# Performance work log

Hardware: AMD Instinct MI355X
Metric: run time of the kernel (lower is better)

## Reference

```python
import jax, jax.numpy as jnp
import numpy as np

B, S, D, H, F, REF = 4, 1024, 512, 8, 2048, 2
HGRID = 32   # sqrt(seq_len)
HALF = 3     # 7x7 window -> half-width 3


def _masks():
    i = jnp.arange(HGRID)
    near = jnp.abs(i[:, None] - i[None, :]) <= HALF            # [h,h]
    inside = (near[:, None, :, None] & near[None, :, None, :]).reshape(S, S)
    # reverse=True mask (mca): outside-window -> -inf, inside -> 0
    m_rev = jnp.where(inside, 0.0, -jnp.inf).astype(jnp.float32)
    # reverse=False mask (msa/nsa): inside-window -> -inf, outside -> 0 (faithful to source)
    m_fwd = jnp.where(inside, -jnp.inf, 0.0).astype(jnp.float32)
    return m_rev, m_fwd


def _mha(q, k, v, w, b, ow, ob, mask):
    # torch nn.MultiheadAttention, batch_first, eval mode (no dropout)
    hd = D // H
    wq, wk, wv = jnp.split(w, 3, axis=0)
    bq, bk, bv = jnp.split(b, 3)

    def proj(t, wt, bt):
        Bt, Lt = t.shape[0], t.shape[1]
        return (t @ wt.T + bt).reshape(Bt, Lt, H, hd).transpose(0, 2, 1, 3)

    qh, kh, vh = proj(q, wq, bq), proj(k, wk, bk), proj(v, wv, bv)
    scores = jnp.einsum('bhqd,bhkd->bhqk', qh, kh) / jnp.sqrt(jnp.float32(hd))
    if mask is not None:
        scores = scores + mask
    a = jax.nn.softmax(scores, axis=-1)
    o = jnp.einsum('bhqk,bhkd->bhqd', a, vh).transpose(0, 2, 1, 3).reshape(q.shape[0], q.shape[1], D)
    return o @ ow.T + ob


def _ln(x, g, b, eps=1e-5):
    m = x.mean(-1, keepdims=True)
    v = ((x - m) ** 2).mean(-1, keepdims=True)
    return (x - m) / jnp.sqrt(v + eps) * g + b


def setup_inputs() -> dict:
    key = jax.random.key(0)
    ks = jax.random.split(key, 16)
    d = {}
    d['x'] = jax.random.normal(ks[0], (B, S, D), jnp.float32)
    d['ref_mca'] = jax.random.normal(ks[1], (B, REF * S, D), jnp.float32)
    d['gate'] = jax.random.uniform(ks[2], (B, S, 5), jnp.float32)
    i = 3
    for p in ['mca', 'ca', 'msa', 'nsa', 'sa']:
        d[p + '_w'] = 0.02 * jax.random.normal(ks[i], (3 * D, D), jnp.float32); i += 1
        d[p + '_b'] = jnp.zeros((3 * D,), jnp.float32)
        d[p + '_ow'] = 0.02 * jax.random.normal(ks[i], (D, D), jnp.float32); i += 1
        d[p + '_ob'] = jnp.zeros((D,), jnp.float32)
    d['ln1_g'] = jnp.ones((D,), jnp.float32); d['ln1_b'] = jnp.zeros((D,), jnp.float32)
    d['ln2_g'] = jnp.ones((D,), jnp.float32); d['ln2_b'] = jnp.zeros((D,), jnp.float32)
    d['fc1_w'] = 0.02 * jax.random.normal(ks[i], (F, D), jnp.float32); i += 1
    d['fc1_b'] = jnp.zeros((F,), jnp.float32)
    d['fc2_w'] = 0.02 * jax.random.normal(ks[i], (D, F), jnp.float32); i += 1
    d['fc2_b'] = jnp.zeros((D,), jnp.float32)
    return d


def reference(x, ref_mca, gate,
              mca_w, mca_b, mca_ow, mca_ob,
              ca_w, ca_b, ca_ow, ca_ob,
              msa_w, msa_b, msa_ow, msa_ob,
              nsa_w, nsa_b, nsa_ow, nsa_ob,
              sa_w, sa_b, sa_ow, sa_ob,
              ln1_g, ln1_b, ln2_g, ln2_b,
              fc1_w, fc1_b, fc2_w, fc2_b):
    m_rev, m_fwd = _masks()
    # mca branch: sum attention over each seq_len chunk of ref_mca (window-inside mask)
    mca_x = jnp.zeros_like(x)
    for r in range(REF):
        chunk = ref_mca[:, r * S:(r + 1) * S, :]
        mca_x = mca_x + _mha(x, chunk, chunk, mca_w, mca_b, mca_ow, mca_ob, m_rev)
    # faithful to source: loop variable leaks, so ca/nsa use the LAST chunk
    ref_last = ref_mca[:, (REF - 1) * S:, :]
    new_x = gate[:, :, 0:1] * mca_x
    new_x = new_x + gate[:, :, 1:2] * _mha(x, ref_last, ref_last, ca_w, ca_b, ca_ow, ca_ob, None)
    new_x = new_x + gate[:, :, 2:3] * _mha(x, x, x, msa_w, msa_b, msa_ow, msa_ob, m_fwd)
    new_x = new_x + gate[:, :, 3:4] * _mha(x, ref_last, x, nsa_w, nsa_b, nsa_ow, nsa_ob, m_fwd)
    new_x = new_x + gate[:, :, 4:5] * _mha(x, x, x, sa_w, sa_b, sa_ow, sa_ob, None)
    h = _ln(new_x, ln1_g, ln1_b)
    y = jax.nn.gelu(h @ fc1_w.T + fc1_b, approximate=False) @ fc2_w.T + fc2_b
    return _ln(h + y, ln2_g, ln2_b)
```

## Files before the change

### kernel.cpp

```cpp
#include <hip/hip_runtime.h>

typedef __bf16 bf16_t;
typedef bf16_t bf16x8 __attribute__((ext_vector_type(8)));
typedef float f32x4v __attribute__((ext_vector_type(4)));
typedef unsigned int u32;

__device__ __forceinline__ void gload16(const bf16_t* g, bf16_t* l) {
    __builtin_amdgcn_global_load_lds((const __attribute__((address_space(1))) u32*)g,
                                     (__attribute__((address_space(3))) u32*)l, 16, 0, 0);
}

struct PackBDesc {
    int nseg;
    int blkOf[21];
    const float* src[20];
    bf16_t* dst[20];
    int chunks[20];
    int dstLd[20];
    int shift[20];
};

__global__ __launch_bounds__(256) void packb_k(PackBDesc d) {
    int b = blockIdx.x;
    int s = 0;
    while (s + 1 < d.nseg && b >= d.blkOf[s + 1]) ++s;
    int idx = (b - d.blkOf[s]) * 256 + threadIdx.x;
    if (idx >= d.chunks[s]) return;
    const float* src = d.src[s] + (size_t)idx * 8;
    int r = idx >> d.shift[s];
    int c8 = idx & ((1 << d.shift[s]) - 1);
    bf16_t* dst = d.dst[s] + (size_t)r * d.dstLd[s] + (size_t)c8 * 8;
    float4 v0 = reinterpret_cast<const float4*>(src)[0];
    float4 v1 = reinterpret_cast<const float4*>(src)[1];
    bf16x8 o;
    o[0] = (bf16_t)v0.x; o[1] = (bf16_t)v0.y; o[2] = (bf16_t)v0.z; o[3] = (bf16_t)v0.w;
    o[4] = (bf16_t)v1.x; o[5] = (bf16_t)v1.y; o[6] = (bf16_t)v1.z; o[7] = (bf16_t)v1.w;
    *reinterpret_cast<bf16x8*>(dst) = o;
}

struct PackFDesc {
    int nseg;
    int blkOf[15];
    const float* src[14];
    float* dst[14];
    int n[14];
};

__global__ __launch_bounds__(256) void packf_k(PackFDesc d) {
    int b = blockIdx.x;
    int s = 0;
    while (s + 1 < d.nseg && b >= d.blkOf[s + 1]) ++s;
    int idx = (b - d.blkOf[s]) * 256 + threadIdx.x;
    if (idx >= d.n[s]) return;
    d.dst[s][idx] = d.src[s][idx];
}

template <int EPI, int BM, int BN>
__device__ __forceinline__ void gemm_core(
    int tm, int tn, int bz,
    const bf16_t* __restrict__ A, int aBS, int aRowOff, int lda,
    const bf16_t* __restrict__ B,
    const float* __restrict__ bias,
    void* __restrict__ Out, int ldo, size_t outSplitStride,
    const float* __restrict__ gate, const float* __restrict__ obcat,
    int kStart, int kLen) {
    constexpr int MB = BM / 32, NB = BN / 32, WM = BM / 2, WN = BN / 2;
    constexpr int CA = BM / 64, CB = BN / 64;
    __shared__ __attribute__((aligned(16))) bf16_t As[2][BM * 32];
    __shared__ __attribute__((aligned(16))) bf16_t Bs[2][BN * 32];
    const int tid = threadIdx.x, lane = tid & 63, w = tid >> 6;
    const int wm = w >> 1, wn = w & 1;
    const int l15 = lane & 15, l16 = lane >> 4;
    const int colS = (lane & 3) * 8, rowS = lane >> 2;

    auto remap = [&](int m) { return (m >> 10) * aBS + aRowOff + (m & 1023); };

    const bf16_t* aS[CA];
    const bf16_t* bS[CB];
#pragma unroll
    for (int c = 0; c < CA; ++c)
        aS[c] = A + (size_t)remap(tm * BM + (CA * w + c) * 16 + rowS) * lda + kStart + colS;
#pragma unroll
    for (int c = 0; c < CB; ++c)
        bS[c] = B + (size_t)(tn * BN + (CB * w + c) * 16 + rowS) * lda + kStart + colS;

    auto stage = [&](int buf, int t) {
        const size_t o = (size_t)t * 32;
#pragma unroll
        for (int c = 0; c < CA; ++c) gload16(aS[c] + o, &As[buf][(CA * w + c) * 512]);
#pragma unroll
        for (int c = 0; c < CB; ++c) gload16(bS[c] + o, &Bs[buf][(CB * w + c) * 512]);
    };

    f32x4v acc[MB][NB] = {};
    const int nt = kLen / 32;
    stage(0, 0);
    __syncthreads();
    int cur = 0;
    for (int t = 0; t < nt; ++t) {
        if (t + 1 < nt) stage(cur ^ 1, t + 1);
        bf16x8 af[MB], bff[NB];
#pragma unroll
        for (int mi = 0; mi < MB; ++mi)
            af[mi] = *reinterpret_cast<const bf16x8*>(&As[cur][(wm * WM + mi * 16 + l15) * 32 + l16 * 8]);
#pragma unroll
        for (int ni = 0; ni < NB; ++ni)
            bff[ni] = *reinterpret_cast<const bf16x8*>(&Bs[cur][(wn * WN + ni * 16 + l15) * 32 + l16 * 8]);
#pragma unroll
        for (int mi = 0; mi < MB; ++mi)
#pragma unroll
            for (int ni = 0; ni < NB; ++ni)
                acc[mi][ni] = __builtin_amdgcn_mfma_f32_16x16x32_bf16(af[mi], bff[ni], acc[mi][ni], 0, 0, 0);
        __syncthreads();
        cur ^= 1;
    }

#pragma unroll
    for (int mi = 0; mi < MB; ++mi) {
#pragma unroll
        for (int ni = 0; ni < NB; ++ni) {
#pragma unroll
            for (int i = 0; i < 4; ++i) {
                int row = tm * BM + wm * WM + mi * 16 + l16 * 4 + i;
                int n = tn * BN + wn * WN + ni * 16 + l15;
                float v = acc[mi][ni][i];
                if (bias && bz == 0) v += bias[n];
                if constexpr (EPI == 0) {
                    ((bf16_t*)Out)[(size_t)row * ldo + n] = (bf16_t)v;
                } else if constexpr (EPI == 1) {
                    float g = 0.5f * v * (1.0f + erff(v * 0.70710678118654752f));
                    ((bf16_t*)Out)[(size_t)row * ldo + n] = (bf16_t)g;
                } else if constexpr (EPI == 3) {
                    ((float*)Out + (size_t)bz * outSplitStride)[(size_t)row * ldo + n] = v;
                } else {
                    if (obcat && bz == 0) {
#pragma unroll
                        for (int p = 0; p < 5; ++p) {
                            float c = (p == 0) ? 2.0f : 1.0f;
                            v += gate[row * 5 + p] * c * obcat[p * 512 + n];
                        }
                    }
                    ((float*)Out + (size_t)bz * outSplitStride)[(size_t)row * ldo + n] = v;
                }
            }
        }
    }
}

struct ProjDesc {
    const bf16_t* A[3];
    int aBS[3], aRowOff[3];
    const bf16_t* B[3];
    const float* bias[3];
    bf16_t* Out[3];
    int ldo[3];
    int ntn[3], base[3];
};

__global__ __launch_bounds__(256) void proj_k(ProjDesc d) {
    int wg = (blockIdx.x & 7) * 272 + (blockIdx.x >> 3);
    int s = (wg >= d.base[2]) ? 2 : (wg >= d.base[1]) ? 1 : 0;
    int local = wg - d.base[s];
    int tn = local % d.ntn[s];
    int tm = local / d.ntn[s];
    gemm_core<0, 128, 128>(tm, tn, 0, d.A[s], d.aBS[s], d.aRowOff[s], 512,
                           d.B[s], d.bias[s], d.Out[s], d.ldo[s], 0, nullptr, nullptr, 0, 512);
}

template <int EPI, int BM, int BN>
__global__ __launch_bounds__(256) void gemmT(
    const bf16_t* __restrict__ A, int aBS, int aRowOff, int lda,
    const bf16_t* __restrict__ B, const float* __restrict__ bias,
    void* __restrict__ Out, int ldo, size_t outSplitStride,
    const float* __restrict__ gate, const float* __restrict__ obcat, int kPerSplit) {
    gemm_core<EPI, BM, BN>(blockIdx.y, blockIdx.x, blockIdx.z, A, aBS, aRowOff, lda, B, bias,
                           Out, ldo, outSplitStride, gate, obcat, blockIdx.z * kPerSplit, kPerSplit);
}

struct AttnDesc {
    const bf16_t* Q[6];
    const bf16_t* K[6];
    const bf16_t* V[6];
    int ldq[6], ldk[6], ldv[6];
    int segOff[6], gidx[6], mask[6];
    bf16_t* acat;
    bf16_t* Op;
    float* Mp;
    float* Lp;
    const float* gate;
};

__global__ __launch_bounds__(512) void attn5_k(AttnDesc d) {
    __shared__ __attribute__((aligned(16))) bf16_t Ks[64][72];
    __shared__ __attribute__((aligned(16))) bf16_t Vt[64][72];
    __shared__ __attribute__((aligned(16))) bf16_t Ps[8][16][40];

    int bid = blockIdx.x;
    int xcd = bid & 7;
    int t = bid >> 3;
    int qt = t / 40;
    int g = (t % 40) * 8 + xcd;
    int u, lg;
    if (g < 32) { u = 0; lg = g; }
    else if (g < 64) { u = 1; lg = g - 32; }
    else if (g < 128) { u = 2; lg = g - 64; }
    else if (g < 192) { u = 3; lg = g - 128; }
    else if (g < 256) { u = 4; lg = g - 192; }
    else { u = 5; lg = g - 256; }
    const bool splitk = (u >= 2);
    const int mask = d.mask[u];
    const int h = lg & 7, z = lg >> 3;
    int b, split;
    if (splitk) { b = z & 3; split = z >> 2; } else { b = z; split = 0; }

    const int tid = threadIdx.x;
    const int lane = tid & 63;
    const int w = tid >> 6;
    const int l15 = lane & 15, l16 = lane >> 4;

    const int qr = qt * 128 + w * 16;
    const int qrow = b * 1024 + qr;
    const int qblk = qr >> 5;
    const int qg = ((w & 1) * 16) + l15;

    const int ldq = d.ldq[u], ldk = d.ldk[u], ldv = d.ldv[u];
    bf16x8 aq[2];
#pragma unroll
    for (int s = 0; s < 2; ++s)
        aq[s] = *reinterpret_cast<const bf16x8*>(
            d.Q[u] + (size_t)(qrow + l15) * ldq + h * 64 + s * 32 + l16 * 8);

    float mrow = -1e30f, lsum = 0.f;
    f32x4v accO[4] = {};

    const int srow = tid >> 3, scol8 = (tid & 7) * 8;
    const int vcol = srow ^ ((tid & 7) << 3);
    const bf16_t* kbase = d.K[u] + (size_t)(b * 1024) * ldk + h * 64 + scol8;
    const bf16_t* vbase = d.V[u] + (size_t)(b * 1024) * ldv + h * 64 + scol8;

    int t0, t1;
    if (splitk) { t0 = split * 8; t1 = t0 + 8; }
    else {
        int klo = qt * 4 - 3; if (klo < 0) klo = 0;
        int khi = qt * 4 + 6; if (khi > 31) khi = 31;
        t0 = klo >> 1; t1 = (khi >> 1) + 1;
    }

    bf16x8 rk, rv, rk2, rv2;
    rk = *reinterpret_cast<const bf16x8*>(kbase + (size_t)(t0 * 64 + srow) * ldk);
    rv = *reinterpret_cast<const bf16x8*>(vbase + (size_t)(t0 * 64 + srow) * ldv);

    for (int tt = t0; tt < t1; ++tt) {
        __syncthreads();
        *reinterpret_cast<bf16x8*>(&Ks[srow][scol8]) = rk;
#pragma unroll
        for (int j = 0; j < 8; ++j) Vt[scol8 + j][vcol] = rv[j];
        if (tt + 1 < t1) {
            rk2 = *reinterpret_cast<const bf16x8*>(kbase + (size_t)((tt + 1) * 64 + srow) * ldk);
            rv2 = *reinterpret_cast<const bf16x8*>(vbase + (size_t)((tt + 1) * 64 + srow) * ldv);
        }
        __syncthreads();

        int bd0 = qblk - tt * 2;     if (bd0 < 0) bd0 = -bd0;
        int bd1 = qblk - tt * 2 - 1; if (bd1 < 0) bd1 = -bd1;
        const bool a0 = (mask != 1) || (bd0 <= 3);
        const bool a1 = (mask != 1) || (bd1 <= 3);
        if (a0 || a1) {
            f32x4v z4[4];
#pragma unroll
            for (int nt = 0; nt < 4; ++nt) {
                bf16x8 kf0 = *reinterpret_cast<const bf16x8*>(&Ks[nt * 16 + l15][l16 * 8]);
                bf16x8 kf1 = *reinterpret_cast<const bf16x8*>(&Ks[nt * 16 + l15][32 + l16 * 8]);
                f32x4v zz = {};
                zz = __builtin_amdgcn_mfma_f32_16x16x32_bf16(kf0, aq[0], zz, 0, 0, 0);
                zz = __builtin_amdgcn_mfma_f32_16x16x32_bf16(kf1, aq[1], zz, 0, 0, 0);
                z4[nt] = zz;
            }
            float p[4][4];
#pragma unroll
            for (int nt = 0; nt < 4; ++nt) {
                const int bd = (nt >> 1) ? bd1 : bd0;
                const bool act = (nt >> 1) ? a1 : a0;
                const bool needMask = (mask == 1) || (mask == 2 && bd <= 3);
#pragma unroll
                for (int i = 0; i < 4; ++i) {
                    float v = z4[nt][i] * 0.125f;
                    if (!act) v = -1e30f;
                    else if (needMask) {
                        int k5 = (nt & 1) * 16 + l16 * 4 + i;
                        int dq = qg - k5; if (dq < 0) dq = -dq;
                        bool inside = (bd <= 3) && (dq <= 3);
                        if (mask == 1 ? !inside : inside) v = -1e30f;
                    }
                    p[nt][i] = v;
                }
            }
            float tmx = p[0][0];
#pragma unroll
            for (int nt = 0; nt < 4; ++nt)
#pragma unroll
                for (int i = 0; i < 4; ++i) tmx = fmaxf(tmx, p[nt][i]);
            tmx = fmaxf(tmx, __shfl_xor(tmx, 16, 64));
            tmx = fmaxf(tmx, __shfl_xor(tmx, 32, 64));
            float mn = fmaxf(mrow, tmx);
            float fac = __expf(mrow - mn);
            mrow = mn;
            float rs = 0.f;
#pragma unroll
            for (int nt = 0; nt < 4; ++nt)
#pragma unroll
                for (int i = 0; i < 4; ++i) {
                    p[nt][i] = __expf(p[nt][i] - mn);
                    rs += p[nt][i];
                }
            rs += __shfl_xor(rs, 16, 64);
            rs += __shfl_xor(rs, 32, 64);
            lsum = lsum * fac + rs;

            float facq[4];
#pragma unroll
            for (int i = 0; i < 4; ++i) facq[i] = __shfl(fac, l16 * 4 + i, 64);
#pragma unroll
            for (int dblk = 0; dblk < 4; ++dblk)
#pragma unroll
                for (int i = 0; i < 4; ++i) accO[dblk][i] *= facq[i];

#pragma unroll
            for (int kh = 0; kh < 2; ++kh) {
#pragma unroll
                for (int n = 0; n < 2; ++n)
#pragma unroll
                    for (int i = 0; i < 4; ++i)
                        Ps[w][l15][n * 16 + l16 * 4 + i] = (bf16_t)p[kh * 2 + n][i];
                bf16x8 pa = *reinterpret_cast<const bf16x8*>(&Ps[w][l15][l16 * 8]);
#pragma unroll
                for (int dblk = 0; dblk < 4; ++dblk) {
                    int dd = dblk * 16 + l15;
                    int csw = ((kh * 4 + l16) ^ (dd >> 3)) * 8;
                    bf16x8 bv = *reinterpret_cast<const bf16x8*>(&Vt[dd][csw]);
                    accO[dblk] = __builtin_amdgcn_mfma_f32_16x16x32_bf16(pa, bv, accO[dblk], 0, 0, 0);
                }
            }
        }
        rk = rk2; rv = rv2;
    }

    if (!splitk) {
        float inv = 1.0f / lsum;
        float invq[4];
#pragma unroll
        for (int i = 0; i < 4; ++i) invq[i] = __shfl(inv, l16 * 4 + i, 64);
#pragma unroll
        for (int dblk = 0; dblk < 4; ++dblk)
#pragma unroll
            for (int i = 0; i < 4; ++i) {
                float gg = d.gate[(size_t)(qrow + l16 * 4 + i) * 5 + d.gidx[u]];
                d.acat[(size_t)(qrow + l16 * 4 + i) * 3072 + d.segOff[u] + h * 64 + dblk * 16 + l15] =
                    (bf16_t)(accO[dblk][i] * invq[i] * gg);
            }
    } else {
        const int su = u - 2;
        bf16_t* Opu = d.Op + (size_t)su * 65536 * 64;
        float* Mpu = d.Mp + su * 65536;
        float* Lpu = d.Lp + su * 65536;
        int pb = ((split * 4 + b) * 8 + h) * 1024 + qr;
        if (l16 == 0) { Mpu[pb + l15] = mrow; Lpu[pb + l15] = lsum; }
#pragma unroll
        for (int dblk = 0; dblk < 4; ++dblk)
#pragma unroll
            for (int i = 0; i < 4; ++i) {
                float gg = d.gate[(size_t)(qrow + l16 * 4 + i) * 5 + d.gidx[u]];
                Opu[(size_t)(pb + l16 * 4 + i) * 64 + dblk * 16 + l15] = (bf16_t)(accO[dblk][i] * gg);
            }
    }
}

struct MergeDesc {
    const bf16_t* Op;
    const float* Mp;
    const float* Lp;
    bf16_t* acat;
    int segOff[4];
};

__global__ __launch_bounds__(256) void merge4_k(MergeDesc d) {
    int u = blockIdx.x >> 10;
    int idx = (blockIdx.x & 1023) * 256 + threadIdx.x;
    const bf16_t* Opu = d.Op + (size_t)u * 65536 * 64;
    const float* Mpu = d.Mp + u * 65536;
    const float* Lpu = d.Lp + u * 65536;
    int dg = idx & 7;
    int q = (idx >> 3) & 1023;
    int h = (idx >> 13) & 7;
    int b = idx >> 16;
    int r0 = ((0 * 4 + b) * 8 + h) * 1024 + q;
    int r1 = ((1 * 4 + b) * 8 + h) * 1024 + q;
    float m0 = Mpu[r0], m1 = Mpu[r1], l0 = Lpu[r0], l1 = Lpu[r1];
    float M = fmaxf(m0, m1);
    float w0 = __expf(m0 - M), w1 = __expf(m1 - M);
    float den = 1.0f / (l0 * w0 + l1 * w1);
    bf16x8 o0 = *reinterpret_cast<const bf16x8*>(Opu + (size_t)r0 * 64 + dg * 8);
    bf16x8 o1 = *reinterpret_cast<const bf16x8*>(Opu + (size_t)r1 * 64 + dg * 8);
    bf16x8 o;
#pragma unroll
    for (int j = 0; j < 8; ++j)
        o[j] = (bf16_t)(((float)o0[j] * w0 + (float)o1[j] * w1) * den);
    *reinterpret_cast<bf16x8*>(d.acat + (size_t)(b * 1024 + q) * 3072 + d.segOff[u] + h * 64 + dg * 8) = o;
}

__global__ __launch_bounds__(256) void ln_k(const float* __restrict__ in0,
                                            const float* __restrict__ in1,
                                            const float* __restrict__ in2,
                                            const float* __restrict__ g,
                                            const float* __restrict__ bb,
                                            float* __restrict__ outf,
                                            bf16_t* __restrict__ outb) {
    __shared__ float red[8];
    int row = blockIdx.x;
    int t = threadIdx.x;
    float x0 = in0[(size_t)row * 512 + t];
    float x1 = in0[(size_t)row * 512 + 256 + t];
    if (in1) {
        x0 += in1[(size_t)row * 512 + t];
        x1 += in1[(size_t)row * 512 + 256 + t];
    }
    if (in2) {
        x0 += in2[(size_t)row * 512 + t];
        x1 += in2[(size_t)row * 512 + 256 + t];
    }
    float s = x0 + x1, sq = x0 * x0 + x1 * x1;
#pragma unroll
    for (int d = 1; d < 64; d <<= 1) {
        s += __shfl_xor(s, d, 64);
        sq += __shfl_xor(sq, d, 64);
    }
    int w = t >> 6;
    if ((t & 63) == 0) { red[w] = s; red[4 + w] = sq; }
    __syncthreads();
    s = red[0] + red[1] + red[2] + red[3];
    sq = red[4] + red[5] + red[6] + red[7];
    float mean = s * (1.0f / 512.0f);
    float var = sq * (1.0f / 512.0f) - mean * mean;
    float rstd = rsqrtf(var + 1e-5f);
    float y0 = (x0 - mean) * rstd * g[t] + bb[t];
    float y1 = (x1 - mean) * rstd * g[256 + t] + bb[256 + t];
    if (outf) {
        outf[(size_t)row * 512 + t] = y0;
        outf[(size_t)row * 512 + 256 + t] = y1;
    }
    if (outb) {
        outb[(size_t)row * 512 + t] = (bf16_t)y0;
        outb[(size_t)row * 512 + 256 + t] = (bf16_t)y1;
    }
}

extern "C" void kernel_launch(void* const* d_in, const int* in_sizes, int n_in,
                              void* d_out, int out_size, void* d_ws, size_t ws_size,
                              hipStream_t stream) {
    (void)in_sizes; (void)n_in; (void)out_size; (void)ws_size;
    const float* x       = (const float*)d_in[0];
    const float* ref_mca = (const float*)d_in[1];
    const float* gate    = (const float*)d_in[2];
    const float *w[5], *wb[5], *ow[5], *ob[5];
    for (int p = 0; p < 5; ++p) {
        w[p]  = (const float*)d_in[3 + p * 4];
        wb[p] = (const float*)d_in[4 + p * 4];
        ow[p] = (const float*)d_in[5 + p * 4];
        ob[p] = (const float*)d_in[6 + p * 4];
    }
    const float* ln1_g = (const float*)d_in[23];
    const float* ln1_b = (const float*)d_in[24];
    const float* ln2_g = (const float*)d_in[25];
    const float* ln2_b = (const float*)d_in[26];
    const float* fc1_w = (const float*)d_in[27];
    const float* fc1_b = (const float*)d_in[28];
    const float* fc2_w = (const float*)d_in[29];
    const float* fc2_b = (const float*)d_in[30];

    char* ws = (char*)d_ws;
    size_t off = 0;
    auto alloc = [&](size_t bytes) {
        char* p = ws + off;
        off += (bytes + 255) & ~(size_t)255;
        return p;
    };
    const size_t S2 = (size_t)4096 * 512;
    bf16_t* xb    = (bf16_t*)alloc(S2 * 2);
    bf16_t* refb  = (bf16_t*)alloc((size_t)8192 * 512 * 2);
    bf16_t* Wxp   = (bf16_t*)alloc((size_t)5120 * 512 * 2);
    bf16_t* WRp   = (bf16_t*)alloc((size_t)2560 * 512 * 2);
    bf16_t* Wop   = (bf16_t*)alloc((size_t)512 * 3072 * 2);
    bf16_t* fc1p  = (bf16_t*)alloc((size_t)2048 * 512 * 2);
    bf16_t* fc2p  = (bf16_t*)alloc((size_t)512 * 2048 * 2);
    float*  bxp   = (float*)alloc((size_t)5120 * 4);
    float*  brp   = (float*)alloc((size_t)2560 * 4);
    float*  obc   = (float*)alloc((size_t)5 * 512 * 4);
    bf16_t* XP    = (bf16_t*)alloc((size_t)4096 * 5120 * 2);
    bf16_t* RP    = (bf16_t*)alloc((size_t)4096 * 2560 * 2);
    bf16_t* R0    = (bf16_t*)alloc((size_t)4096 * 1024 * 2);
    bf16_t* acat  = (bf16_t*)alloc((size_t)4096 * 3072 * 2);
    float*  newx  = (float*)alloc(S2 * 4 * 2);
    float*  hbuf  = (float*)alloc(S2 * 4);
    bf16_t* Opart = (bf16_t*)alloc((size_t)4 * 65536 * 64 * 2);
    float*  Mpart = (float*)alloc((size_t)4 * 65536 * 4);
    float*  Lpart = (float*)alloc((size_t)4 * 65536 * 4);
    bf16_t* hb  = refb;
    bf16_t* ub  = XP;
    float*  yp  = newx;

    PackBDesc pb{};
    int nb = 0, blk = 0;
    auto addB = [&](const float* s, bf16_t* dptr, int chunks, int dstLd, int shift) {
        pb.src[nb] = s; pb.dst[nb] = dptr; pb.chunks[nb] = chunks;
        pb.dstLd[nb] = dstLd; pb.shift[nb] = shift;
        pb.blkOf[nb] = blk; blk += (chunks + 255) / 256; ++nb;
    };
    auto addLin = [&](const float* s, bf16_t* dptr, long elems) {
        addB(s, dptr, (int)(elems / 8), 0, 30);
    };
    addLin(x, xb, (long)4096 * 512);
    addLin(ref_mca, refb, (long)8192 * 512);
    addLin(w[0], Wxp, (long)512 * 512);
    addLin(w[1], Wxp + (size_t)512 * 512, (long)512 * 512);
    addLin(w[2], Wxp + (size_t)1024 * 512, (long)1536 * 512);
    addLin(w[3], Wxp + (size_t)2560 * 512, (long)512 * 512);
    addLin(w[3] + (size_t)1024 * 512, Wxp + (size_t)3072 * 512, (long)512 * 512);
    addLin(w[4], Wxp + (size_t)3584 * 512, (long)1536 * 512);
    addLin(w[0] + (size_t)512 * 512, WRp, (long)1024 * 512);
    addLin(w[1] + (size_t)512 * 512, WRp + (size_t)1024 * 512, (long)1024 * 512);
    addLin(w[3] + (size_t)512 * 512, WRp + (size_t)2048 * 512, (long)512 * 512);
    const float* owSeg[6] = {ow[0], ow[0], ow[1], ow[2], ow[3], ow[4]};
    for (int s = 0; s < 6; ++s)
        addB(owSeg[s], Wop + (size_t)s * 512, 32768, 3072, 6);
    addLin(fc1_w, fc1p, (long)2048 * 512);
    addLin(fc2_w, fc2p, (long)512 * 2048);
    pb.nseg = nb; pb.blkOf[nb] = blk;
    packb_k<<<blk, 256, 0, stream>>>(pb);

    PackFDesc pf{};
    int nf = 0, fblk = 0;
    auto addF = [&](const float* s, float* dptr, int n) {
        pf.src[nf] = s; pf.dst[nf] = dptr; pf.n[nf] = n;
        pf.blkOf[nf] = fblk; fblk += (n + 255) / 256; ++nf;
    };
    addF(wb[0], bxp, 512);
    addF(wb[1], bxp + 512, 512);
    addF(wb[2], bxp + 1024, 1536);
    addF(wb[3], bxp + 2560, 512);
    addF(wb[3] + 1024, bxp + 3072, 512);
    addF(wb[4], bxp + 3584, 1536);
    addF(wb[0] + 512, brp, 1024);
    addF(wb[1] + 512, brp + 1024, 1024);
    addF(wb[3] + 512, brp + 2048, 512);
    for (int p = 0; p < 5; ++p) addF(ob[p], obc + p * 512, 512);
    pf.nseg = nf; pf.blkOf[nf] = fblk;
    packf_k<<<fblk, 256, 0, stream>>>(pf);

    ProjDesc pd{};
    pd.A[0] = xb;   pd.aBS[0] = 1024; pd.aRowOff[0] = 0;    pd.B[0] = Wxp; pd.bias[0] = bxp; pd.Out[0] = XP; pd.ldo[0] = 5120; pd.ntn[0] = 40;
    pd.A[1] = refb; pd.aBS[1] = 2048; pd.aRowOff[1] = 1024; pd.B[1] = WRp; pd.bias[1] = brp; pd.Out[1] = RP; pd.ldo[1] = 2560; pd.ntn[1] = 20;
    pd.A[2] = refb; pd.aBS[2] = 2048; pd.aRowOff[2] = 0;    pd.B[2] = WRp; pd.bias[2] = brp; pd.Out[2] = R0; pd.ldo[2] = 1024; pd.ntn[2] = 8;
    pd.base[0] = 0; pd.base[1] = 40 * 32; pd.base[2] = 40 * 32 + 20 * 32;
    proj_k<<<(40 + 20 + 8) * 32, 256, 0, stream>>>(pd);

    AttnDesc ad{};
    auto setU = [&](int u, const bf16_t* Q, int lq, const bf16_t* K, int lk,
                    const bf16_t* V, int lv, int seg, int gi, int mk) {
        ad.Q[u] = Q; ad.ldq[u] = lq; ad.K[u] = K; ad.ldk[u] = lk; ad.V[u] = V; ad.ldv[u] = lv;
        ad.segOff[u] = seg; ad.gidx[u] = gi; ad.mask[u] = mk;
    };
    setU(0, XP, 5120, R0, 1024, R0 + 512, 1024, 0, 0, 1);
    setU(1, XP, 5120, RP, 2560, RP + 512, 2560, 512, 0, 1);
    setU(2, XP + 512, 5120, RP + 1024, 2560, RP + 1536, 2560, 1024, 1, 0);
    setU(3, XP + 1024, 5120, XP + 1536, 5120, XP + 2048, 5120, 1536, 2, 2);
    setU(4, XP + 2560, 5120, RP + 2048, 2560, XP + 3072, 5120, 2048, 3, 2);
    setU(5, XP + 3584, 5120, XP + 4096, 5120, XP + 4608, 5120, 2560, 4, 0);
    ad.acat = acat; ad.Op = Opart; ad.Mp = Mpart; ad.Lp = Lpart; ad.gate = gate;
    attn5_k<<<2560, 512, 0, stream>>>(ad);

    MergeDesc md{};
    md.Op = Opart; md.Mp = Mpart; md.Lp = Lpart; md.acat = acat;
    md.segOff[0] = 1024; md.segOff[1] = 1536; md.segOff[2] = 2048; md.segOff[3] = 2560;
    merge4_k<<<4096, 256, 0, stream>>>(md);

    gemmT<4, 64, 64><<<dim3(8, 64, 2), 256, 0, stream>>>(acat, 1024, 0, 3072, Wop, nullptr,
                                                         newx, 512, S2, gate, obc, 1536);
    ln_k<<<4096, 256, 0, stream>>>(newx, newx + S2, nullptr, ln1_g, ln1_b, hbuf, hb);
    gemmT<1, 128, 128><<<dim3(16, 32, 1), 256, 0, stream>>>(hb, 1024, 0, 512, fc1p, fc1_b,
                                                            ub, 2048, 0, nullptr, nullptr, 512);
    gemmT<3, 64, 64><<<dim3(8, 64, 2), 256, 0, stream>>>(ub, 1024, 0, 2048, fc2p, fc2_b,
                                                         yp, 512, S2, nullptr, nullptr, 1024);
    ln_k<<<4096, 256, 0, stream>>>(hbuf, yp, yp + S2, ln2_g, ln2_b, (float*)d_out, nullptr);
}
```

Measured before the change: 324.9 us.

## Fold softmax scale and log2e into Q projection, lazy rescale, exp2

Multiplies the Q projection outputs by 0.125*log2(e) in the GEMM epilogue, selected per column tile by a mask, so attention scores come out already in the base-2 domain. Attention then uses exp2f instead of __expf and skips the per-tile multiply. Online-softmax rescaling of the accumulator runs only when some row's max grows by more than 8, which removes shuffles and multiplies on most tiles. The attention block-index mapping also drops the XCD-aware swizzle in favour of a plain modulo. The lazy threshold keeps exponent values up to 2^8, and storing pre-scaled Q in bf16 adds a little rounding error.

```diff
diff --git a/kernel.cpp b/kernel.cpp
--- a/kernel.cpp
+++ b/kernel.cpp
@@ -4,11 +4,14 @@
 typedef bf16_t bf16x8 __attribute__((ext_vector_type(8)));
 typedef float f32x4v __attribute__((ext_vector_type(4)));
 typedef unsigned int u32;
+typedef unsigned long long u64;
 
 __device__ __forceinline__ void gload16(const bf16_t* g, bf16_t* l) {
     __builtin_amdgcn_global_load_lds((const __attribute__((address_space(1))) u32*)g,
                                      (__attribute__((address_space(3))) u32*)l, 16, 0, 0);
 }
+
+#define QSCALE 0.18033688011112042f
 
 struct PackBDesc {
     int nseg;
@@ -63,7 +66,7 @@
     const float* __restrict__ bias,
     void* __restrict__ Out, int ldo, size_t outSplitStride,
     const float* __restrict__ gate, const float* __restrict__ obcat,
-    int kStart, int kLen) {
+    int kStart, int kLen, u64 scaleMask) {
     constexpr int MB = BM / 32, NB = BN / 32, WM = BM / 2, WN = BN / 2;
     constexpr int CA = BM / 64, CB = BN / 64;
     __shared__ __attribute__((aligned(16))) bf16_t As[2][BM * 32];
@@ -115,6 +118,7 @@
         cur ^= 1;
     }
 
+    const bool doScale = (EPI == 0) && ((scaleMask >> tn) & 1ULL);
 #pragma unroll
     for (int mi = 0; mi < MB; ++mi) {
 #pragma unroll
@@ -126,6 +130,7 @@
                 float v = acc[mi][ni][i];
                 if (bias && bz == 0) v += bias[n];
                 if constexpr (EPI == 0) {
+                    if (doScale) v *= QSCALE;
                     ((bf16_t*)Out)[(size_t)row * ldo + n] = (bf16_t)v;
                 } else if constexpr (EPI == 1) {
                     float g = 0.5f * v * (1.0f + erff(v * 0.70710678118654752f));
@@ -155,6 +160,7 @@
     bf16_t* Out[3];
     int ldo[3];
     int ntn[3], base[3];
+    u64 qmask[3];
 };
 
 __global__ __launch_bounds__(256) void proj_k(ProjDesc d) {
@@ -164,7 +170,8 @@
     int tn = local % d.ntn[s];
     int tm = local / d.ntn[s];
     gemm_core<0, 128, 128>(tm, tn, 0, d.A[s], d.aBS[s], d.aRowOff[s], 512,
-                           d.B[s], d.bias[s], d.Out[s], d.ldo[s], 0, nullptr, nullptr, 0, 512);
+                           d.B[s], d.bias[s], d.Out[s], d.ldo[s], 0, nullptr, nullptr, 0, 512,
+                           d.qmask[s]);
 }
 
 template <int EPI, int BM, int BN>
@@ -174,7 +181,7 @@
     void* __restrict__ Out, int ldo, size_t outSplitStride,
     const float* __restrict__ gate, const float* __restrict__ obcat, int kPerSplit) {
     gemm_core<EPI, BM, BN>(blockIdx.y, blockIdx.x, blockIdx.z, A, aBS, aRowOff, lda, B, bias,
-                           Out, ldo, outSplitStride, gate, obcat, blockIdx.z * kPerSplit, kPerSplit);
+                           Out, ldo, outSplitStride, gate, obcat, blockIdx.z * kPerSplit, kPerSplit, 0);
 }
 
 struct AttnDesc {
@@ -196,10 +203,8 @@
     __shared__ __attribute__((aligned(16))) bf16_t Ps[8][16][40];
 
     int bid = blockIdx.x;
-    int xcd = bid & 7;
-    int t = bid >> 3;
-    int qt = t / 40;
-    int g = (t % 40) * 8 + xcd;
+    int g = bid % 320;
+    int qt = bid / 320;
     int u, lg;
     if (g < 32) { u = 0; lg = g; }
     else if (g < 64) { u = 1; lg = g - 32; }
@@ -284,7 +289,7 @@
                 const bool needMask = (mask == 1) || (mask == 2 && bd <= 3);
 #pragma unroll
                 for (int i = 0; i < 4; ++i) {
-                    float v = z4[nt][i] * 0.125f;
+                    float v = z4[nt][i];
                     if (!act) v = -1e30f;
                     else if (needMask) {
                         int k5 = (nt & 1) * 16 + l16 * 4 + i;
@@ -302,28 +307,30 @@
                 for (int i = 0; i < 4; ++i) tmx = fmaxf(tmx, p[nt][i]);
             tmx = fmaxf(tmx, __shfl_xor(tmx, 16, 64));
             tmx = fmaxf(tmx, __shfl_xor(tmx, 32, 64));
-            float mn = fmaxf(mrow, tmx);
-            float fac = __expf(mrow - mn);
-            mrow = mn;
+            if (!__all(tmx - mrow <= 8.0f)) {
+                float mn = fmaxf(mrow, tmx);
+                float fac = exp2f(mrow - mn);
+                mrow = mn;
+                lsum *= fac;
+                float facq[4];
+#pragma unroll
+                for (int i = 0; i < 4; ++i) facq[i] = __shfl(fac, l16 * 4 + i, 64);
+#pragma unroll
+                for (int dblk = 0; dblk < 4; ++dblk)
+#pragma unroll
+                    for (int i = 0; i < 4; ++i) accO[dblk][i] *= facq[i];
+            }
             float rs = 0.f;
 #pragma unroll
             for (int nt = 0; nt < 4; ++nt)
 #pragma unroll
                 for (int i = 0; i < 4; ++i) {
-                    p[nt][i] = __expf(p[nt][i] - mn);
+                    p[nt][i] = exp2f(p[nt][i] - mrow);
                     rs += p[nt][i];
                 }
             rs += __shfl_xor(rs, 16, 64);
             rs += __shfl_xor(rs, 32, 64);
-            lsum = lsum * fac + rs;
-
-            float facq[4];
-#pragma unroll
-            for (int i = 0; i < 4; ++i) facq[i] = __shfl(fac, l16 * 4 + i, 64);
-#pragma unroll
-            for (int dblk = 0; dblk < 4; ++dblk)
-#pragma unroll
-                for (int i = 0; i < 4; ++i) accO[dblk][i] *= facq[i];
+            lsum += rs;
 
 #pragma unroll
             for (int kh = 0; kh < 2; ++kh) {
@@ -397,7 +404,7 @@
     int r1 = ((1 * 4 + b) * 8 + h) * 1024 + q;
     float m0 = Mpu[r0], m1 = Mpu[r1], l0 = Lpu[r0], l1 = Lpu[r1];
     float M = fmaxf(m0, m1);
-    float w0 = __expf(m0 - M), w1 = __expf(m1 - M);
+    float w0 = exp2f(m0 - M), w1 = exp2f(m1 - M);
     float den = 1.0f / (l0 * w0 + l1 * w1);
     bf16x8 o0 = *reinterpret_cast<const bf16x8*>(Opu + (size_t)r0 * 64 + dg * 8);
     bf16x8 o1 = *reinterpret_cast<const bf16x8*>(Opu + (size_t)r1 * 64 + dg * 8);
@@ -561,6 +568,7 @@
     pd.A[1] = refb; pd.aBS[1] = 2048; pd.aRowOff[1] = 1024; pd.B[1] = WRp; pd.bias[1] = brp; pd.Out[1] = RP; pd.ldo[1] = 2560; pd.ntn[1] = 20;
     pd.A[2] = refb; pd.aBS[2] = 2048; pd.aRowOff[2] = 0;    pd.B[2] = WRp; pd.bias[2] = brp; pd.Out[2] = R0; pd.ldo[2] = 1024; pd.ntn[2] = 8;
     pd.base[0] = 0; pd.base[1] = 40 * 32; pd.base[2] = 40 * 32 + 20 * 32;
+    pd.qmask[0] = 0xF0F00FFFULL; pd.qmask[1] = 0; pd.qmask[2] = 0;
     proj_k<<<(40 + 20 + 8) * 32, 256, 0, stream>>>(pd);
 
     AttnDesc ad{};
```

Result: no change. 320.5 us (-1.3%).
